# Performance work log

Measured on AMD Instinct MI355X. Metric: run time of the kernel, lower is better.

## Reference

```python
import jax, jax.numpy as jnp
import numpy as np

ALPHA, BETA, INIT_P = 100.0, 1000.0, 2.0
K_NEIGHBORS = 24


def index_points(pts, idx):
    # pts: [B,N,C], idx: [B,...] int -> [B,...,C]
    B = pts.shape[0]
    b = jnp.arange(B).reshape((B,) + (1,) * (idx.ndim - 1))
    return pts[b, idx]


def fps(xyz, m):
    # furthest point sampling, deterministic start at index 0. xyz: [B,N,3]
    B, N, _ = xyz.shape
    def step(carry, _):
        dist, far = carry
        centroid = xyz[jnp.arange(B), far]              # [B,3]
        d = jnp.sum((xyz - centroid[:, None, :]) ** 2, -1)
        dist = jnp.minimum(dist, d)
        nxt = jnp.argmax(dist, -1).astype(jnp.int32)
        return (dist, nxt), far
    init = (jnp.full((B, N), 1e10, xyz.dtype), jnp.zeros((B,), jnp.int32))
    _, idx = jax.lax.scan(step, init, None, length=m)
    return idx.T                                        # [B,m]


def knn_indices(k, xyz, centers):
    # squared distances [B,G,N], k smallest
    d = (jnp.sum(centers ** 2, -1)[..., None]
         - 2.0 * jnp.einsum('bgc,bnc->bgn', centers, xyz)
         + jnp.sum(xyz ** 2, -1)[:, None, :])
    _, idx = jax.lax.top_k(-d, k)
    return idx                                          # [B,G,K]


def normalize(x, ref):
    # torch: mean = ref.unsqueeze(-2); std over ALL elements of (x-mean), ddof=1
    d = x - ref[..., None, :]
    std = jnp.std(d, ddof=1)
    return d / (std + 1e-5)


def fourier_map(t, Bmat):
    # t: [B,7,G,K]; Bmat: [7, C//2] (already includes scale) -> [B,C,G,K]
    x = jnp.transpose(t, (0, 2, 3, 1))                  # [B,G,K,7]
    proj = 2.0 * jnp.pi * (x @ Bmat)                    # [B,G,K,C/2]
    f = jnp.concatenate([jnp.sin(proj), jnp.cos(proj)], -1)
    f = jnp.sign(f) * jnp.abs(f) ** 5
    return jnp.transpose(f, (0, 3, 1, 2))


def tr_embed(my_dim, t):
    # t: [B,3,G,K] -> [B,my_dim,G,K]
    B, C, G, K = t.shape
    F = my_dim // (2 * C)
    dim_embed = ALPHA ** (jnp.arange(F, dtype=t.dtype) / F)
    div = BETA * t[..., None] / dim_embed               # [B,3,G,K,F]
    pe = jnp.stack([jnp.sin(div), jnp.cos(div)], -1).reshape(B, C, G, K, 2 * F)
    pe = jnp.transpose(pe, (0, 1, 4, 2, 3)).reshape(B, my_dim, G, K)
    return pe


def lga(lc_xyz, lc_x, knn_xyz, knn_x, Bmat):
    B, G, K, C = knn_x.shape
    knn_x = normalize(knn_x, lc_x)
    knn_xyz = normalize(knn_xyz, lc_xyz)
    lc_rep = jnp.transpose(jnp.broadcast_to(lc_xyz[:, :, None, :], (B, G, K, 3)), (0, 3, 1, 2))
    knn_xyz_t = jnp.transpose(knn_xyz, (0, 3, 1, 2))    # [B,3,G,K]
    knn_x_t = jnp.transpose(knn_x, (0, 3, 1, 2))        # [B,C,G,K]
    cross = jnp.cross(knn_xyz_t, lc_rep, axis=1)
    dot = jnp.sum(knn_xyz_t * lc_rep, 1, keepdims=True)
    emb_in = jnp.concatenate([knn_xyz_t, cross, dot], 1)  # [B,7,G,K]
    emb = fourier_map(emb_in, Bmat)                       # [B,C,G,K]
    knn_x_w = jnp.concatenate([knn_x_t, emb], 1)          # [B,2C,G,K]
    pe = tr_embed(2 * C, knn_xyz_t) + tr_embed(2 * C, lc_rep)
    return (knn_x_w + pe) * pe


def k_anp(x):
    # x: [B,2C,G,K], data-dependent p-norm attention over K
    std = jnp.std(x, axis=-1, ddof=1, keepdims=True)
    p = jax.lax.stop_gradient(INIT_P + jnp.log1p(std.mean()))  # torch uses .item()
    norm = jnp.sum(jnp.abs(x) ** p, -1, keepdims=True) ** (1.0 / p)
    lc = norm / (norm + 1e-8)
    e = jnp.exp(lc)
    return (x * e).mean(-1) / e.mean(-1)                # [B,2C,G]


def bn_gelu(x, gamma, beta):
    # BatchNorm1d in training mode (batch stats, biased var) + exact GELU
    mean = x.mean((0, 2), keepdims=True)
    var = ((x - mean) ** 2).mean((0, 2), keepdims=True)
    y = (x - mean) / jnp.sqrt(var + 1e-5) * gamma[None, :, None] + beta[None, :, None]
    return jax.nn.gelu(y, approximate=False)


def stage(xyz, x, group_num, Bmat, gamma, beta):
    # xyz: [B,N,3]; x: [B,C,N]
    feats = jnp.transpose(x, (0, 2, 1))
    fi = fps(xyz, group_num)
    lc_xyz = index_points(xyz, fi)
    lc_x = index_points(feats, fi)
    ki = knn_indices(K_NEIGHBORS, xyz, lc_xyz)
    knn_xyz = index_points(xyz, ki)
    knn_x = index_points(feats, ki)
    w = lga(lc_xyz, lc_x, knn_xyz, knn_x, Bmat)
    pooled = k_anp(w) + w.mean(-1)                      # [B,2C,G]
    return lc_xyz, bn_gelu(pooled, gamma, beta)


def setup_inputs() -> dict:
    key = jax.random.key(0)
    k1, k2, k3, k4 = jax.random.split(key, 4)
    B, N, C0 = 4, 4096, 72
    return {
        'xyz': jax.random.uniform(k1, (B, N, 3), jnp.float32),
        'x': jax.random.normal(k2, (B, C0, N), jnp.float32),
        'fourier_B0': jax.random.normal(k3, (7, C0 // 2), jnp.float32) * 50.0,
        'fourier_B1': jax.random.normal(k4, (7, C0), jnp.float32) * 50.0,
        'bn_gamma0': jnp.ones((2 * C0,), jnp.float32),
        'bn_beta0': jnp.zeros((2 * C0,), jnp.float32),
        'bn_gamma1': jnp.ones((4 * C0,), jnp.float32),
        'bn_beta1': jnp.zeros((4 * C0,), jnp.float32),
    }


def reference(xyz, x, fourier_B0, fourier_B1, bn_gamma0, bn_beta0, bn_gamma1, bn_beta1):
    N = xyz.shape[1]
    xyz, x = stage(xyz, x, N // 2, fourier_B0, bn_gamma0, bn_beta0)   # -> [B,144,2048]
    xyz, x = stage(xyz, x, N // 4, fourier_B1, bn_gamma1, bn_beta1)   # -> [B,288,1024]
    return x
```

## Files before the change

kernel.cpp:

```cpp
#include <hip/hip_runtime.h>
#include <math.h>

#define KNB 24

typedef float v2f __attribute__((ext_vector_type(2)));

template<int CTRL>
__device__ __forceinline__ float dppmax(float v) {
    int t = __builtin_amdgcn_update_dpp(0, __float_as_int(v), CTRL, 0xf, 0xf, true);
    return fmaxf(v, __int_as_float(t));
}
template<int CTRL>
__device__ __forceinline__ unsigned dppmaxu(unsigned v) {
    unsigned t = (unsigned)__builtin_amdgcn_update_dpp(0, (int)v, CTRL, 0xf, 0xf, true);
    return v > t ? v : t;
}
template<int CTRL>
__device__ __forceinline__ double dppmax64(double v) {
    unsigned long long u = __double_as_longlong(v);
    int lo = (int)(unsigned)(u & 0xffffffffull);
    int hi = (int)(unsigned)(u >> 32);
    int tlo = __builtin_amdgcn_update_dpp(0, lo, CTRL, 0xf, 0xf, true);
    int thi = __builtin_amdgcn_update_dpp(0, hi, CTRL, 0xf, 0xf, true);
    double t = __longlong_as_double(((unsigned long long)(unsigned)thi << 32) | (unsigned)tlo);
    return __builtin_fmax(v, t);
}

template<int NPT, int NWAVE>
__global__ __launch_bounds__(64 * NWAVE, 1) void k_fps_tr(const float* __restrict__ xyz,
                                                          int* __restrict__ fi,
                                                          int N, int M,
                                                          const float* __restrict__ x0,
                                                          float* __restrict__ feats,
                                                          int C, int NT, int nT, int cT) {
#pragma clang fp contract(off)
    const int NP2 = NPT / 2;
    const int tid = threadIdx.x;
    extern __shared__ char smc[];

    if ((int)blockIdx.x >= 4) {
        int bid = blockIdx.x - 4;
        int tilesPerB = nT * cT;
        int b = bid / tilesPerB;
        int t2 = bid - b * tilesPerB;
        int cTile = t2 / nT;
        int nTile = t2 - cTile * nT;
        int tx = tid & 31, ty = tid >> 5;
        const int ROWS = 2 * NWAVE;
        float* tile = (float*)smc;
        for (int r = ty; r < 32; r += ROWS) {
            int c = cTile * 32 + r, n = nTile * 32 + tx;
            if (c < C && n < NT) tile[r * 33 + tx] = x0[((size_t)b * C + c) * NT + n];
        }
        __syncthreads();
        for (int r = ty; r < 32; r += ROWS) {
            int n = nTile * 32 + r, c = cTile * 32 + tx;
            if (c < C && n < NT) feats[((size_t)b * NT + n) * C + c] = tile[tx * 33 + r];
        }
        return;
    }

    const int b = blockIdx.x;
    const int lane = tid & 63;
    const int wid = tid >> 6;
    unsigned long long* keys = (unsigned long long*)smc;
    int* fi_lds = (int*)(smc + 2 * NWAVE * 8);
    size_t poff = ((size_t)(2 * NWAVE * 8) + (size_t)M * 4 + 15) & ~(size_t)15;
    float4* pts = (float4*)(smc + poff);

    const float* p = xyz + (size_t)b * N * 3;
    for (int i = tid; i < N; i += 64 * NWAVE)
        pts[i] = make_float4(p[i*3], p[i*3+1], p[i*3+2], 0.0f);
    __syncthreads();

    const int base = tid * NPT;
    v2f rx[NP2], ry[NP2], rz[NP2], dist[NP2];
    unsigned lowc[NPT];
#pragma unroll
    for (int j = 0; j < NP2; ++j) {
        int i0 = base + 2 * j, i1 = base + 2 * j + 1;
        rx[j] = (v2f){p[i0*3],   p[i1*3]};
        ry[j] = (v2f){p[i0*3+1], p[i1*3+1]};
        rz[j] = (v2f){p[i0*3+2], p[i1*3+2]};
        dist[j] = (v2f){1e10f, 1e10f};
        lowc[2*j]   = ~(unsigned)i0;
        lowc[2*j+1] = ~(unsigned)i1;
    }

    int far = 0;
    float cx = p[0], cy = p[1], cz = p[2];
    for (int it = 0; it < M; ++it) {
        if (tid == 0) fi_lds[it] = far;
        v2f cx2 = (v2f){cx, cx}, cy2 = (v2f){cy, cy}, cz2 = (v2f){cz, cz};
        double kA = 0.0, kB = 0.0;
#pragma unroll
        for (int j = 0; j < NP2; ++j) {
            v2f dx = rx[j] - cx2, dy = ry[j] - cy2, dz = rz[j] - cz2;
            v2f d = (dx*dx + dy*dy) + dz*dz;
            v2f dd = __builtin_elementwise_min(dist[j], d);
            dist[j] = dd;
            double k0 = __longlong_as_double(
                ((unsigned long long)__float_as_uint(dd.x) << 32) | lowc[2*j]);
            double k1 = __longlong_as_double(
                ((unsigned long long)__float_as_uint(dd.y) << 32) | lowc[2*j+1]);
            kA = __builtin_fmax(kA, k0);
            kB = __builtin_fmax(kB, k1);
        }
        double km = __builtin_fmax(kA, kB);
        km = dppmax64<0x111>(km); km = dppmax64<0x112>(km);
        km = dppmax64<0x114>(km); km = dppmax64<0x118>(km);
        km = dppmax64<0x142>(km); km = dppmax64<0x143>(km);
        if (lane == 63) keys[(it & 1) * NWAVE + wid] = __double_as_longlong(km);
        __syncthreads();
        const unsigned long long* kk = keys + (it & 1) * NWAVE;
        double g;
        if (NWAVE == 8) {
            double m0 = __builtin_fmax(__longlong_as_double((long long)kk[0]),
                                       __longlong_as_double((long long)kk[1]));
            double m1 = __builtin_fmax(__longlong_as_double((long long)kk[2]),
                                       __longlong_as_double((long long)kk[3]));
            double m2 = __builtin_fmax(__longlong_as_double((long long)kk[4]),
                                       __longlong_as_double((long long)kk[5]));
            double m3 = __builtin_fmax(__longlong_as_double((long long)kk[6]),
                                       __longlong_as_double((long long)kk[7]));
            g = __builtin_fmax(__builtin_fmax(m0, m1), __builtin_fmax(m2, m3));
        } else {
            g = __longlong_as_double((long long)kk[0]);
#pragma unroll
            for (int w = 1; w < NWAVE; ++w)
                g = __builtin_fmax(g, __longlong_as_double((long long)kk[w]));
        }
        far = (int)(~(unsigned)__double_as_longlong(g));
        float4 c = pts[far];
        cx = c.x; cy = c.y; cz = c.z;
    }
    __syncthreads();
    for (int i = tid; i < M; i += 64 * NWAVE) fi[b * M + i] = fi_lds[i];
}

template<int NPT>
__global__ __launch_bounds__(256) void k_knn_t(const float* __restrict__ xyz,
                                               const float* __restrict__ feats,
                                               const int* __restrict__ fi,
                                               float* __restrict__ lc_xyz,
                                               float* __restrict__ lc_x,
                                               int* __restrict__ ki,
                                               double* __restrict__ part,
                                               int B, int N, int G, int C, int identity) {
#pragma clang fp contract(off)
    int bg = blockIdx.x; int b = bg / G; int g = bg % G;
    int idx = identity ? g : fi[bg];
    const int tid = threadIdx.x;
    const int lane = tid & 63;
    const int wid = tid >> 6;
    __shared__ unsigned long long keys[2][4];
    __shared__ int kis[KNB];
    __shared__ float cfeat[144];
    const float* p = xyz + (size_t)b * N * 3;
    float cx = p[idx*3], cy = p[idx*3+1], cz = p[idx*3+2];
    if (tid < 3) lc_xyz[(size_t)bg * 3 + tid] = p[idx*3 + tid];
    for (int c = tid; c < C; c += 256) {
        float v = feats[((size_t)b * N + idx) * C + c];
        lc_x[(size_t)bg * C + c] = v;
        cfeat[c] = v;
    }
    float cc = (cx*cx + cy*cy) + cz*cz;
    const int base = tid * NPT;
    float dist[NPT];
#pragma unroll
    for (int j = 0; j < NPT; ++j) {
        float x0 = p[(base+j)*3], x1 = p[(base+j)*3+1], x2 = p[(base+j)*3+2];
        float xx = (x0*x0 + x1*x1) + x2*x2;
        float dt = (cx*x0 + cy*x1) + cz*x2;
        dist[j] = (cc - 2.0f*dt) + xx;
    }
    for (int kk = 0; kk < KNB; ++kk) {
        float bv = 1e30f;
#pragma unroll
        for (int j = 0; j < NPT; ++j) bv = fminf(bv, dist[j]);
        int lj = 0;
#pragma unroll
        for (int j = NPT - 1; j >= 0; --j) if (dist[j] == bv) lj = j;
        unsigned ub = ~__float_as_uint(bv);
        unsigned r = ub;
        r = dppmaxu<0x111>(r); r = dppmaxu<0x112>(r);
        r = dppmaxu<0x114>(r); r = dppmaxu<0x118>(r);
        r = dppmaxu<0x142>(r); r = dppmaxu<0x143>(r);
        unsigned uwin = (unsigned)__builtin_amdgcn_readlane((int)r, 63);
        unsigned long long mask = __ballot(ub == uwin);
        int src = __builtin_ctzll(mask);
        int gi = __builtin_amdgcn_readlane(base + lj, src);
        unsigned long long key = ((unsigned long long)uwin << 32) | (unsigned)(~gi);
        if (lane == 0) keys[kk & 1][wid] = key;
        __syncthreads();
        unsigned long long k0 = keys[kk & 1][0];
#pragma unroll
        for (int w = 1; w < 4; ++w) {
            unsigned long long kw = keys[kk & 1][w];
            if (kw > k0) k0 = kw;
        }
        int win = (int)(~(unsigned)k0);
        if (tid == 0) kis[kk] = win;
        if (win >= base && win < base + NPT) {
            int wj = win - base;
#pragma unroll
            for (int j = 0; j < NPT; ++j) if (j == wj) dist[j] = 1e30f;
        }
    }
    __syncthreads();
    if (tid < KNB) ki[(size_t)bg * KNB + tid] = kis[tid];
    double s = 0.0, s2 = 0.0, s3 = 0.0, s4 = 0.0;
    for (int i = tid; i < KNB * C; i += 256) {
        int k = i / C, c = i - k * C;
        float d = feats[((size_t)b * N + kis[k]) * C + c] - cfeat[c];
        s += (double)d; s2 += (double)d * (double)d;
    }
    if (tid < KNB * 3) {
        int k = tid / 3, c = tid - k * 3;
        float ctr = (c == 0) ? cx : ((c == 1) ? cy : cz);
        float d = p[kis[k] * 3 + c] - ctr;
        s3 += (double)d; s4 += (double)d * (double)d;
    }
    for (int off = 32; off > 0; off >>= 1) {
        s += __shfl_down(s, off); s2 += __shfl_down(s2, off);
        s3 += __shfl_down(s3, off); s4 += __shfl_down(s4, off);
    }
    __shared__ double sw[4][4];
    if ((tid & 63) == 0) {
        sw[wid][0] = s; sw[wid][1] = s2; sw[wid][2] = s3; sw[wid][3] = s4;
    }
    __syncthreads();
    if (tid == 0) {
        double t0 = 0.0, t1 = 0.0, t2 = 0.0, t3 = 0.0;
        for (int w = 0; w < 4; ++w) {
            t0 += sw[w][0]; t1 += sw[w][1]; t2 += sw[w][2]; t3 += sw[w][3];
        }
        double* q = part + (size_t)bg * 4;
        q[0] = t0; q[1] = t1; q[2] = t2; q[3] = t3;
    }
}

__global__ __launch_bounds__(1024) void k_reduce(const double* __restrict__ part,
                                                 double* __restrict__ acc, int n) {
    double s0 = 0.0, s1 = 0.0, s2 = 0.0, s3 = 0.0;
    for (int i = threadIdx.x; i < n; i += 1024) {
        const double* q = part + (size_t)i * 4;
        s0 += q[0]; s1 += q[1]; s2 += q[2]; s3 += q[3];
    }
    for (int off = 32; off > 0; off >>= 1) {
        s0 += __shfl_down(s0, off); s1 += __shfl_down(s1, off);
        s2 += __shfl_down(s2, off); s3 += __shfl_down(s3, off);
    }
    __shared__ double sw[16][4];
    int wid = threadIdx.x >> 6;
    if ((threadIdx.x & 63) == 0) {
        sw[wid][0] = s0; sw[wid][1] = s1; sw[wid][2] = s2; sw[wid][3] = s3;
    }
    __syncthreads();
    if (threadIdx.x == 0) {
        double t0 = 0.0, t1 = 0.0, t2 = 0.0, t3 = 0.0;
        for (int w = 0; w < 16; ++w) {
            t0 += sw[w][0]; t1 += sw[w][1]; t2 += sw[w][2]; t3 += sw[w][3];
        }
        acc[0] = t0; acc[1] = t1; acc[2] = t2; acc[3] = t3;
    }
}

__global__ __launch_bounds__(256) void k_feature(
    const float* __restrict__ xyz, const float* __restrict__ feats,
    const float* __restrict__ lc_xyz, const float* __restrict__ lc_x,
    const int* __restrict__ ki, const float* __restrict__ Bmat,
    const double* __restrict__ accp, float* __restrict__ pooled,
    int B, int N, int G, int C, double nx, double nz)
{
    int bg = blockIdx.x; int b = bg / G; int g = bg % G;
    int tid = threadIdx.x;
    int C2 = C >> 1;
    int Cout = 2 * C;
    int F = C / 3;
    extern __shared__ float sm[];
    float* t7    = sm;
    float* sxyzn = t7 + KNB * 7;
    int*   kidx  = (int*)(sxyzn + KNB * 3);
    float* semb  = (float*)(kidx + KNB);
    float* sfeat = semb + KNB * C;

    double a0 = accp[0], a1 = accp[1], a2 = accp[2], a3 = accp[3];
    double vx = (a1 - a0 * a0 / nx) / (nx - 1.0);
    float invx = 1.0f / (sqrtf((float)vx) + 1e-5f);
    double vz = (a3 - a2 * a2 / nz) / (nz - 1.0);
    float invz = 1.0f / (sqrtf((float)vz) + 1e-5f);

    float l0 = lc_xyz[(size_t)bg*3], l1 = lc_xyz[(size_t)bg*3+1], l2 = lc_xyz[(size_t)bg*3+2];

    if (tid < KNB) {
        int idx = ki[(size_t)bg * KNB + tid];
        kidx[tid] = idx;
        const float* q = xyz + ((size_t)b * N + idx) * 3;
        float a0f = (q[0]-l0)*invz, a1f = (q[1]-l1)*invz, a2f = (q[2]-l2)*invz;
        float c0 = a1f*l2 - a2f*l1;
        float c1 = a2f*l0 - a0f*l2;
        float c2 = a0f*l1 - a1f*l0;
        float dt = (a0f*l0 + a1f*l1) + a2f*l2;
        float* tp = t7 + tid * 7;
        tp[0]=a0f; tp[1]=a1f; tp[2]=a2f; tp[3]=c0; tp[4]=c1; tp[5]=c2; tp[6]=dt;
        sxyzn[tid*3]=a0f; sxyzn[tid*3+1]=a1f; sxyzn[tid*3+2]=a2f;
    }
    __syncthreads();
    for (int i = tid; i < KNB * C; i += blockDim.x) {
        int k = i / C, c = i - k * C;
        sfeat[i] = feats[((size_t)b * N + kidx[k]) * C + c];
    }
    const float TWO_PI = 6.2831854820251465f;
    for (int i = tid; i < KNB * C2; i += blockDim.x) {
        int k = i / C2, m2 = i % C2;
        const float* tp = t7 + k * 7;
        float s = 0.0f;
        for (int j = 0; j < 7; ++j) s += tp[j] * Bmat[j * C2 + m2];
        float pr = TWO_PI * s;
        float sn, cs;
        __sincosf(pr, &sn, &cs);
        float sn2 = sn*sn, cs2 = cs*cs;
        semb[k*C + m2]      = sn2*sn2*sn;
        semb[k*C + C2 + m2] = cs2*cs2*cs;
    }
    __syncthreads();
    for (int m = tid; m < Cout; m += blockDim.x) {
        int c3 = m / (2 * F);
        int r  = m % (2 * F);
        int f  = r >> 1;
        int trig = r & 1;
        float de = __powf(100.0f, (float)f / (float)F);
        float rde = 1000.0f / de;
        float lv = (c3 == 0) ? l0 : ((c3 == 1) ? l1 : l2);
        float a2v = lv * rde;
        float pe2 = trig ? __cosf(a2v) : __sinf(a2v);
        float lfm = (m < C) ? lc_x[(size_t)bg * C + m] : 0.0f;
        float acc = 0.0f;
        for (int k = 0; k < KNB; ++k) {
            float v;
            if (m < C) {
                v = (sfeat[k * C + m] - lfm) * invx;
            } else {
                v = semb[k * C + (m - C)];
            }
            float a1v = sxyzn[k*3 + c3] * rde;
            float pe1 = trig ? __cosf(a1v) : __sinf(a1v);
            float pe = pe1 + pe2;
            acc += (v + pe) * pe;
        }
        float mean = acc / 24.0f;
        pooled[((size_t)b * Cout + m) * G + g] = 2.0f * mean;
    }
}

__global__ __launch_bounds__(256) void k_bn(const float* __restrict__ pooled,
                                            const float* __restrict__ gamma,
                                            const float* __restrict__ beta,
                                            float* __restrict__ out,
                                            int B, int Cout, int G, int transposed) {
    int m = blockIdx.x;
    double s = 0.0, s2 = 0.0;
    for (int i = threadIdx.x; i < B * G; i += 256) {
        int b = i / G, g = i % G;
        float v = pooled[((size_t)b * Cout + m) * G + g];
        s += (double)v; s2 += (double)v * (double)v;
    }
    for (int off = 32; off > 0; off >>= 1) { s += __shfl_down(s, off); s2 += __shfl_down(s2, off); }
    __shared__ double sw[4], sw2[4];
    __shared__ float smv[2];
    int wid = threadIdx.x >> 6;
    if ((threadIdx.x & 63) == 0) { sw[wid] = s; sw2[wid] = s2; }
    __syncthreads();
    if (threadIdx.x == 0) {
        double ts = sw[0] + sw[1] + sw[2] + sw[3];
        double ts2 = sw2[0] + sw2[1] + sw2[2] + sw2[3];
        double n = (double)(B * G);
        double mean = ts / n;
        double var = ts2 / n - mean * mean;
        smv[0] = (float)mean; smv[1] = (float)var;
    }
    __syncthreads();
    float mean = smv[0], var = smv[1];
    float ga = gamma[m], be = beta[m];
    for (int i = threadIdx.x; i < B * G; i += 256) {
        int b = i / G, g = i % G;
        float v = pooled[((size_t)b * Cout + m) * G + g];
        float y = (v - mean) / sqrtf(var + 1e-5f) * ga + be;
        float ge = 0.5f * y * (1.0f + erff(y / 1.4142135381698608f));
        if (transposed) out[((size_t)b * G + g) * Cout + m] = ge;
        else            out[((size_t)b * Cout + m) * G + g] = ge;
    }
}

extern "C" void kernel_launch(void* const* d_in, const int* in_sizes, int n_in,
                              void* d_out, int out_size, void* d_ws, size_t ws_size,
                              hipStream_t stream) {
    const int B = 4, N1 = 4096, C0 = 72, G1 = 2048, Co1 = 144;
    const int N2 = 2048, C1 = 144, G2 = 1024, Co2 = 288;

    const float* xyz = (const float*)d_in[0];
    const float* x0  = (const float*)d_in[1];
    const float* B0  = (const float*)d_in[2];
    const float* B1  = (const float*)d_in[3];
    const float* g0  = (const float*)d_in[4];
    const float* be0 = (const float*)d_in[5];
    const float* g1  = (const float*)d_in[6];
    const float* be1 = (const float*)d_in[7];
    float* out = (float*)d_out;

    char* wp = (char*)d_ws;
    size_t off = 0;
    auto A = [&](size_t bytes) -> void* {
        void* p = wp + off;
        off += (bytes + 255) & ~(size_t)255;
        return p;
    };
    float* feats1  = (float*)A((size_t)B*N1*C0*4);
    int*   fi1     = (int*)  A((size_t)B*G1*4);
    float* lcx1    = (float*)A((size_t)B*G1*3*4);
    float* lcf1    = (float*)A((size_t)B*G1*C0*4);
    int*   ki1     = (int*)  A((size_t)B*G1*KNB*4);
    double* acc    = (double*)A(8*8);
    double* part   = (double*)A((size_t)B*G1*4*8);
    float* pooled1 = (float*)A((size_t)B*Co1*G1*4);
    float* feats2  = (float*)A((size_t)B*N2*C1*4);
    float* lcx2    = (float*)A((size_t)B*G2*3*4);
    float* lcf2    = lcf1;
    int*   ki2     = ki1;
    float* pooled2 = feats1;

    {
        const int nT = N1 / 32, cT = (C0 + 31) / 32;
        const int NW = 8;
        size_t poff = ((size_t)(2*NW*8) + (size_t)G1*4 + 15) & ~(size_t)15;
        size_t shm = poff + (size_t)N1*16;
        k_fps_tr<8, NW><<<B + B*nT*cT, 64*NW, shm, stream>>>(xyz, fi1, N1, G1,
                                                             x0, feats1, C0, N1, nT, cT);
    }
    k_knn_t<16><<<B*G1, 256, 0, stream>>>(xyz, feats1, fi1, lcx1, lcf1, ki1, part,
                                          B, N1, G1, C0, 0);
    k_reduce<<<1, 1024, 0, stream>>>(part, acc, B*G1);
    {
        size_t shf = (size_t)(KNB*7 + KNB*3 + KNB + 2*KNB*C0) * 4;
        k_feature<<<B*G1, 256, shf, stream>>>(xyz, feats1, lcx1, lcf1, ki1, B0, acc, pooled1,
                                              B, N1, G1, C0,
                                              (double)B*G1*KNB*C0, (double)B*G1*KNB*3);
    }
    k_bn<<<Co1, 256, 0, stream>>>(pooled1, g0, be0, feats2, B, Co1, G1, 1);

    k_knn_t<8><<<B*G2, 256, 0, stream>>>(lcx1, feats2, (const int*)nullptr,
                                         lcx2, lcf2, ki2, part, B, N2, G2, C1, 1);
    k_reduce<<<1, 1024, 0, stream>>>(part, acc + 4, B*G2);
    {
        size_t shf = (size_t)(KNB*7 + KNB*3 + KNB + 2*KNB*C1) * 4;
        k_feature<<<B*G2, 256, shf, stream>>>(lcx1, feats2, lcx2, lcf2, ki2, B1, acc + 4, pooled2,
                                              B, N2, G2, C1,
                                              (double)B*G2*KNB*C1, (double)B*G2*KNB*3);
    }
    k_bn<<<Co2, 256, 0, stream>>>(pooled2, g1, be1, out, B, Co2, G2, 0);
}
```

Before: 1.613 ms.

## Stream FPS point coordinates from LDS in SoA layout with fewer waves

FPS now holds per-thread point coordinates in a lane-interleaved SoA buffer in shared memory and reads them each iteration, instead of keeping them in registers. The block shrinks from 8 waves with 8 points per thread to 4 waves with 16 points per thread, so the cross-wave reduction after each barrier is shorter. The centroid lookup also reads from the same SoA buffer. The aim is lower barrier and reduction cost per iteration, at the price of three extra LDS loads per point pair every iteration.

```diff
diff --git a/kernel.cpp b/kernel.cpp
--- a/kernel.cpp
+++ b/kernel.cpp
@@ -35,6 +35,7 @@
                                                           int C, int NT, int nT, int cT) {
 #pragma clang fp contract(off)
     const int NP2 = NPT / 2;
+    const int LANES = 64 * NWAVE;
     const int tid = threadIdx.x;
     extern __shared__ char smc[];
 
@@ -63,28 +64,31 @@
     const int b = blockIdx.x;
     const int lane = tid & 63;
     const int wid = tid >> 6;
-    unsigned long long* keys = (unsigned long long*)smc;
-    int* fi_lds = (int*)(smc + 2 * NWAVE * 8);
-    size_t poff = ((size_t)(2 * NWAVE * 8) + (size_t)M * 4 + 15) & ~(size_t)15;
-    float4* pts = (float4*)(smc + poff);
+    const int CB_BYTES = 3 * NP2 * LANES * 8;
+    v2f* cbuf = (v2f*)smc;
+    unsigned long long* keys = (unsigned long long*)(smc + CB_BYTES);
+    int* fi_lds = (int*)(smc + CB_BYTES + 2 * NWAVE * 8);
 
     const float* p = xyz + (size_t)b * N * 3;
-    for (int i = tid; i < N; i += 64 * NWAVE)
-        pts[i] = make_float4(p[i*3], p[i*3+1], p[i*3+2], 0.0f);
+    {
+        float* cb = (float*)smc;
+        for (int i = tid; i < N; i += LANES) {
+            int l = i / NPT, s = i % NPT, j2 = s >> 1, h = s & 1;
+#pragma unroll
+            for (int c = 0; c < 3; ++c)
+                cb[((c * NP2 + j2) * LANES + l) * 2 + h] = p[i * 3 + c];
+        }
+    }
     __syncthreads();
 
     const int base = tid * NPT;
-    v2f rx[NP2], ry[NP2], rz[NP2], dist[NP2];
+    v2f dist[NP2];
     unsigned lowc[NPT];
 #pragma unroll
     for (int j = 0; j < NP2; ++j) {
-        int i0 = base + 2 * j, i1 = base + 2 * j + 1;
-        rx[j] = (v2f){p[i0*3],   p[i1*3]};
-        ry[j] = (v2f){p[i0*3+1], p[i1*3+1]};
-        rz[j] = (v2f){p[i0*3+2], p[i1*3+2]};
         dist[j] = (v2f){1e10f, 1e10f};
-        lowc[2*j]   = ~(unsigned)i0;
-        lowc[2*j+1] = ~(unsigned)i1;
+        lowc[2*j]   = ~(unsigned)(base + 2*j);
+        lowc[2*j+1] = ~(unsigned)(base + 2*j + 1);
     }
 
     int far = 0;
@@ -94,15 +98,18 @@
         v2f cx2 = (v2f){cx, cx}, cy2 = (v2f){cy, cy}, cz2 = (v2f){cz, cz};
         double kA = 0.0, kB = 0.0;
 #pragma unroll
-        for (int j = 0; j < NP2; ++j) {
-            v2f dx = rx[j] - cx2, dy = ry[j] - cy2, dz = rz[j] - cz2;
+        for (int j2 = 0; j2 < NP2; ++j2) {
+            v2f xx = cbuf[(0 * NP2 + j2) * LANES + tid];
+            v2f yy = cbuf[(1 * NP2 + j2) * LANES + tid];
+            v2f zz = cbuf[(2 * NP2 + j2) * LANES + tid];
+            v2f dx = xx - cx2, dy = yy - cy2, dz = zz - cz2;
             v2f d = (dx*dx + dy*dy) + dz*dz;
-            v2f dd = __builtin_elementwise_min(dist[j], d);
-            dist[j] = dd;
+            v2f dd = __builtin_elementwise_min(dist[j2], d);
+            dist[j2] = dd;
             double k0 = __longlong_as_double(
-                ((unsigned long long)__float_as_uint(dd.x) << 32) | lowc[2*j]);
+                ((unsigned long long)__float_as_uint(dd.x) << 32) | lowc[2*j2]);
             double k1 = __longlong_as_double(
-                ((unsigned long long)__float_as_uint(dd.y) << 32) | lowc[2*j+1]);
+                ((unsigned long long)__float_as_uint(dd.y) << 32) | lowc[2*j2+1]);
             kA = __builtin_fmax(kA, k0);
             kB = __builtin_fmax(kB, k1);
         }
@@ -114,16 +121,12 @@
         __syncthreads();
         const unsigned long long* kk = keys + (it & 1) * NWAVE;
         double g;
-        if (NWAVE == 8) {
+        if (NWAVE == 4) {
             double m0 = __builtin_fmax(__longlong_as_double((long long)kk[0]),
                                        __longlong_as_double((long long)kk[1]));
             double m1 = __builtin_fmax(__longlong_as_double((long long)kk[2]),
                                        __longlong_as_double((long long)kk[3]));
-            double m2 = __builtin_fmax(__longlong_as_double((long long)kk[4]),
-                                       __longlong_as_double((long long)kk[5]));
-            double m3 = __builtin_fmax(__longlong_as_double((long long)kk[6]),
-                                       __longlong_as_double((long long)kk[7]));
-            g = __builtin_fmax(__builtin_fmax(m0, m1), __builtin_fmax(m2, m3));
+            g = __builtin_fmax(m0, m1);
         } else {
             g = __longlong_as_double((long long)kk[0]);
 #pragma unroll
@@ -131,11 +134,16 @@
                 g = __builtin_fmax(g, __longlong_as_double((long long)kk[w]));
         }
         far = (int)(~(unsigned)__double_as_longlong(g));
-        float4 c = pts[far];
-        cx = c.x; cy = c.y; cz = c.z;
-    }
-    __syncthreads();
-    for (int i = tid; i < M; i += 64 * NWAVE) fi[b * M + i] = fi_lds[i];
+        {
+            int fl = far / NPT, fs = far % NPT, fj2 = fs >> 1, fh = fs & 1;
+            const float* cb = (const float*)smc;
+            cx = cb[((0 * NP2 + fj2) * LANES + fl) * 2 + fh];
+            cy = cb[((1 * NP2 + fj2) * LANES + fl) * 2 + fh];
+            cz = cb[((2 * NP2 + fj2) * LANES + fl) * 2 + fh];
+        }
+    }
+    __syncthreads();
+    for (int i = tid; i < M; i += LANES) fi[b * M + i] = fi_lds[i];
 }
 
 template<int NPT>
@@ -432,11 +440,10 @@
 
     {
         const int nT = N1 / 32, cT = (C0 + 31) / 32;
-        const int NW = 8;
-        size_t poff = ((size_t)(2*NW*8) + (size_t)G1*4 + 15) & ~(size_t)15;
-        size_t shm = poff + (size_t)N1*16;
-        k_fps_tr<8, NW><<<B + B*nT*cT, 64*NW, shm, stream>>>(xyz, fi1, N1, G1,
-                                                             x0, feats1, C0, N1, nT, cT);
+        const int NW = 4, NPT = 16, NP2 = NPT / 2, LANES = 64 * NW;
+        size_t shm = (size_t)(3 * NP2 * LANES * 8) + (size_t)(2 * NW * 8) + (size_t)G1 * 4;
+        k_fps_tr<NPT, NW><<<B + B*nT*cT, 64*NW, shm, stream>>>(xyz, fi1, N1, G1,
+                                                               x0, feats1, C0, N1, nT, cT);
     }
     k_knn_t<16><<<B*G1, 256, 0, stream>>>(xyz, feats1, fi1, lcx1, lcf1, ki1, part,
                                           B, N1, G1, C0, 0);
```

New measurement: 1.788 ms. +10.9%, slower.
